# Performance work log

Measured on AMD Instinct MI355X. Metric: run time of the kernel, lower is better.

The kernel has to match this reference:

```python
import jax, jax.numpy as jnp
import numpy as np

B, L_VLM, L_EXP = 4, 768, 64
L_TOT = L_VLM + L_EXP
D_VLM, D_EXP = 2048, 1024
H, DH = 8, 256
ROPE_BASE = 10000.0
SCALE = 1.0 / np.sqrt(DH).astype(np.float32)


def setup_inputs() -> dict:
    key = jax.random.key(0)
    ks = jax.random.split(key, 12)
    s = 0.02  # weight init scale
    return {
        "vlm_hidden": jax.random.normal(ks[0], (B, L_VLM, D_VLM), jnp.float32),
        "exp_hidden": jax.random.normal(ks[1], (B, L_EXP, D_EXP), jnp.float32),
        "attention_mask": jnp.zeros((B, 1, L_TOT, L_TOT), jnp.float32),  # additive mask
        "position_ids": jnp.broadcast_to(jnp.arange(L_TOT, dtype=jnp.int32)[None, :], (B, L_TOT)),
        "wq_v": jax.random.normal(ks[2], (D_VLM, H * DH), jnp.float32) * s,
        "wk_v": jax.random.normal(ks[3], (D_VLM, H * DH), jnp.float32) * s,
        "wv_v": jax.random.normal(ks[4], (D_VLM, H * DH), jnp.float32) * s,
        "wo_v": jax.random.normal(ks[5], (H * DH, D_VLM), jnp.float32) * s,
        "wq_e": jax.random.normal(ks[6], (D_EXP, H * DH), jnp.float32) * s,
        "wk_e": jax.random.normal(ks[7], (D_EXP, H * DH), jnp.float32) * s,
        "wv_e": jax.random.normal(ks[8], (D_EXP, H * DH), jnp.float32) * s,
        "wo_e": jax.random.normal(ks[9], (H * DH, D_EXP), jnp.float32) * s,
    }


def _proj(hs, w):
    # [B, L, D] @ [D, H*DH] -> [B, H, L, DH]
    b, l, _ = hs.shape
    return jnp.einsum('bld,de->ble', hs, w).reshape(b, l, H, DH).transpose(0, 2, 1, 3)


def _rope(x, cos, sin):
    # NeoX-style rotate-half (Gemma / vLLM RotaryEmbedding with rotary_dim == head_dim)
    d2 = x.shape[-1] // 2
    x1, x2 = x[..., :d2], x[..., d2:]
    return jnp.concatenate([x1 * cos - x2 * sin, x2 * cos + x1 * sin], axis=-1)


def reference(vlm_hidden, exp_hidden, attention_mask, position_ids,
              wq_v, wk_v, wv_v, wo_v, wq_e, wk_e, wv_e, wo_e):
    # 1) separate per-stream Q/K/V projections, 2) concat along sequence dim
    q = jnp.concatenate([_proj(vlm_hidden, wq_v), _proj(exp_hidden, wq_e)], axis=2)
    k = jnp.concatenate([_proj(vlm_hidden, wk_v), _proj(exp_hidden, wk_e)], axis=2)
    v = jnp.concatenate([_proj(vlm_hidden, wv_v), _proj(exp_hidden, wv_e)], axis=2)

    # 3) rotary positional embedding on the joint sequence
    inv_freq = 1.0 / (ROPE_BASE ** (jnp.arange(0, DH, 2, dtype=jnp.float32) / DH))  # [DH/2]
    freqs = position_ids.astype(jnp.float32)[:, :, None] * inv_freq                 # [B, L, DH/2]
    cos = jnp.cos(freqs)[:, None]  # [B, 1, L, DH/2]
    sin = jnp.sin(freqs)[:, None]
    q = _rope(q, cos, sin)
    k = _rope(k, cos, sin)

    # 4) masked attention over the joint sequence
    scores = jnp.einsum('bhqd,bhkd->bhqk', q, k) * SCALE + attention_mask
    probs = jax.nn.softmax(scores, axis=-1)
    out = jnp.einsum('bhqk,bhkd->bhqd', probs, v)              # [B, H, L, DH]
    out = out.transpose(0, 2, 1, 3).reshape(B, L_TOT, H * DH)  # [B, L, H*DH]

    # 5) split back and apply per-stream output projections
    vlm_out = jnp.einsum('ble,ed->bld', out[:, :L_VLM], wo_v)
    exp_out = jnp.einsum('ble,ed->bld', out[:, L_VLM:], wo_e)
    return vlm_out, exp_out
```

## Files before the change

### kernel.cpp

```cpp
#include <hip/hip_runtime.h>

typedef unsigned short u16;
using bf16x8 = __attribute__((ext_vector_type(8))) __bf16;
using f32x4  = __attribute__((ext_vector_type(4))) float;

__device__ __forceinline__ u16 f2bf(float f) {
  unsigned u = __builtin_bit_cast(unsigned, f);
  u += 0x7FFFu + ((u >> 16) & 1u);
  return (u16)(u >> 16);
}
__device__ __forceinline__ float bf2f(u16 s) {
  unsigned u = ((unsigned)s) << 16;
  return __builtin_bit_cast(float, u);
}
__device__ __forceinline__ void lds16(const void* g, void* l) {
  __builtin_amdgcn_global_load_lds(
      (const __attribute__((address_space(1))) void*)g,
      (__attribute__((address_space(3))) void*)l, 16, 0, 0);
}

#define PH_SYNC() \
  __builtin_amdgcn_s_barrier(); \
  asm volatile("s_waitcnt lgkmcnt(0)" ::: "memory"); \
  __builtin_amdgcn_sched_barrier(0);

#define MFMA8(MA, MB) \
  __builtin_amdgcn_s_setprio(1); \
  acc[MA][0] = __builtin_amdgcn_mfma_f32_16x16x32_bf16(a0, b0, acc[MA][0], 0, 0, 0); \
  acc[MB][0] = __builtin_amdgcn_mfma_f32_16x16x32_bf16(a1, b0, acc[MB][0], 0, 0, 0); \
  acc[MA][1] = __builtin_amdgcn_mfma_f32_16x16x32_bf16(a0, b1, acc[MA][1], 0, 0, 0); \
  acc[MB][1] = __builtin_amdgcn_mfma_f32_16x16x32_bf16(a1, b1, acc[MB][1], 0, 0, 0); \
  acc[MA][2] = __builtin_amdgcn_mfma_f32_16x16x32_bf16(a0, b2, acc[MA][2], 0, 0, 0); \
  acc[MB][2] = __builtin_amdgcn_mfma_f32_16x16x32_bf16(a1, b2, acc[MB][2], 0, 0, 0); \
  acc[MA][3] = __builtin_amdgcn_mfma_f32_16x16x32_bf16(a0, b3, acc[MA][3], 0, 0, 0); \
  acc[MB][3] = __builtin_amdgcn_mfma_f32_16x16x32_bf16(a1, b3, acc[MB][3], 0, 0, 0); \
  __builtin_amdgcn_s_setprio(0);

__device__ __forceinline__ void gemm_dp(
    const u16* aR0, const u16* aR1, const u16* bR0, const u16* bR1,
    int NT, int t, u16* As, u16* Bs, f32x4 acc[4][4])
{
  const int lane = t & 63;
  const int fr = lane & 15;
  const int sA = ((lane >> 4) ^ ((fr >> 1) & 3)) << 3;
  const int offA = (((t >> 7) & 1) * 64 + fr) * 32 + sA;
  const int offB = (((t >> 6) & 1) * 64 + fr) * 32 + sA;

  lds16(aR0,      As + t * 8);
  lds16(aR1,      As + 2048 + t * 8);
  lds16(bR0,      Bs + t * 8);
  lds16(bR1,      Bs + 2048 + t * 8);
  lds16(aR0 + 32, As + 4096 + t * 8);
  lds16(aR1 + 32, As + 4096 + 2048 + t * 8);
  lds16(bR0 + 32, Bs + 4096 + t * 8);
  lds16(bR1 + 32, Bs + 4096 + 2048 + t * 8);
  lds16(bR0 + 64, Bs + 8192 + t * 8);
  lds16(bR1 + 64, Bs + 8192 + 2048 + t * 8);
  lds16(aR0 + 64, As + 8192 + t * 8);
  lds16(aR1 + 64, As + 8192 + 2048 + t * 8);
  lds16(bR0 + 96, Bs + 8192 + 4096 + t * 8);
  lds16(bR1 + 96, Bs + 8192 + 4096 + 2048 + t * 8);
  asm volatile("s_waitcnt vmcnt(10)" ::: "memory");
  __builtin_amdgcn_s_barrier();

  for (int T = 0; T < NT; ++T) {
    const int p = T & 1;
    u16* Ab = As + p * 8192;
    u16* Bb = Bs + p * 8192;
    u16* An = As + (p ^ 1) * 8192;
    const bool s1 = (T + 1 < NT), s2 = (T + 2 < NT);
    const int k1 = (T + 1) * 64, k2 = (T + 2) * 64;
    bf16x8 a0, a1, b0, b1, b2, b3;

    a0 = *(const bf16x8*)(Ab + offA);
    a1 = *(const bf16x8*)(Ab + offA + 512);
    b0 = *(const bf16x8*)(Bb + offB);
    b1 = *(const bf16x8*)(Bb + offB + 512);
    b2 = *(const bf16x8*)(Bb + offB + 1024);
    b3 = *(const bf16x8*)(Bb + offB + 1536);
    if (s1) {
      lds16(aR0 + k1 + 32, An + 4096 + t * 8);
      lds16(aR1 + k1 + 32, An + 4096 + 2048 + t * 8);
    }
    PH_SYNC();
    MFMA8(0, 1);
    __builtin_amdgcn_s_barrier();

    a0 = *(const bf16x8*)(Ab + offA + 1024);
    a1 = *(const bf16x8*)(Ab + offA + 1536);
    if (s2) {
      lds16(bR0 + k2, Bb + t * 8);
      lds16(bR1 + k2, Bb + 2048 + t * 8);
    }
    PH_SYNC();
    MFMA8(2, 3);
    if (s2) asm volatile("s_waitcnt vmcnt(10)" ::: "memory");
    else    asm volatile("s_waitcnt vmcnt(0)"  ::: "memory");
    __builtin_amdgcn_s_barrier();

    a0 = *(const bf16x8*)(Ab + offA + 4096);
    a1 = *(const bf16x8*)(Ab + offA + 4096 + 512);
    b0 = *(const bf16x8*)(Bb + offB + 4096);
    b1 = *(const bf16x8*)(Bb + offB + 4096 + 512);
    b2 = *(const bf16x8*)(Bb + offB + 4096 + 1024);
    b3 = *(const bf16x8*)(Bb + offB + 4096 + 1536);
    if (s2) {
      lds16(aR0 + k2, Ab + t * 8);
      lds16(aR1 + k2, Ab + 2048 + t * 8);
    }
    PH_SYNC();
    MFMA8(0, 1);
    __builtin_amdgcn_s_barrier();

    a0 = *(const bf16x8*)(Ab + offA + 4096 + 1024);
    a1 = *(const bf16x8*)(Ab + offA + 4096 + 1536);
    if (s2) {
      lds16(bR0 + k2 + 32, Bb + 4096 + t * 8);
      lds16(bR1 + k2 + 32, Bb + 4096 + 2048 + t * 8);
    }
    PH_SYNC();
    MFMA8(2, 3);
    if (s2) asm volatile("s_waitcnt vmcnt(10)" ::: "memory");
    else    asm volatile("s_waitcnt vmcnt(0)"  ::: "memory");
    __builtin_amdgcn_s_barrier();
  }
}

struct PrepArgs {
  const float* tsrc[8]; u16* tdst[8]; int tK[8]; int tN[8];
  const float* csrc[2]; u16* cdst[2]; int cn4[2];
};

__global__ __launch_bounds__(256) void g_prep(PrepArgs a)
{
  __shared__ float T[32][33];
  const int z = blockIdx.z;
  if (z < 8) {
    const int Krows = a.tK[z], Ncols = a.tN[z];
    const int k0 = blockIdx.y * 32, n0 = blockIdx.x * 32;
    if (k0 >= Krows || n0 >= Ncols) return;
    const float* W = a.tsrc[z];
    u16* Wt = a.tdst[z];
    const int tx = threadIdx.x & 31, ty = threadIdx.x >> 5;
#pragma unroll
    for (int r = 0; r < 4; ++r)
      T[ty + r * 8][tx] = W[(size_t)(k0 + ty + r * 8) * Ncols + n0 + tx];
    __syncthreads();
#pragma unroll
    for (int r = 0; r < 4; ++r)
      Wt[(size_t)(n0 + ty + r * 8) * Krows + k0 + tx] = f2bf(T[tx][ty + r * 8]);
  } else {
    const int j = z - 8;
    const int n4 = a.cn4[j];
    const float* X = a.csrc[j];
    u16* Y = a.cdst[j];
    const int blk = blockIdx.y * gridDim.x + blockIdx.x;
    const int stride = gridDim.x * gridDim.y * 256;
    for (int i = blk * 256 + threadIdx.x; i < n4; i += stride) {
      float4 f = ((const float4*)X)[i];
      ushort4 u;
      u.x = f2bf(f.x); u.y = f2bf(f.y); u.z = f2bf(f.z); u.w = f2bf(f.w);
      ((ushort4*)Y)[i] = u;
    }
  }
}

__global__ __launch_bounds__(256) void g_proj_qkv(
    const u16* __restrict__ Xv, const u16* __restrict__ Xe,
    const u16* __restrict__ Wv_cat, const u16* __restrict__ We_cat,
    u16* __restrict__ Qb, u16* __restrict__ Kb, u16* __restrict__ Vt)
{
  __shared__ __align__(16) u16 As[16384], Bs[16384];
  const int z = blockIdx.z;
  const u16* X; const u16* Wt; int Kdim, rows_pb, l_off;
  if (z == 0) { X = Xv; Wt = Wv_cat; Kdim = 2048; rows_pb = 768; l_off = 0; }
  else {
    if (blockIdx.y >= 2) return;
    X = Xe; Wt = We_cat; Kdim = 1024; rows_pb = 64; l_off = 768;
  }
  const int t = threadIdx.x;
  const int m0 = blockIdx.y * 128, n0 = blockIdx.x * 128;
  const int r0 = t >> 2;
  const int sw = ((t & 3) ^ ((t >> 3) & 3)) * 8;
  const u16* a0 = X + (size_t)(m0 + r0) * Kdim + sw;
  const u16* a1 = X + (size_t)(m0 + r0 + 64) * Kdim + sw;
  const u16* b0 = Wt + (size_t)(n0 + r0) * Kdim + sw;
  const u16* b1 = Wt + (size_t)(n0 + r0 + 64) * Kdim + sw;

  f32x4 acc[4][4] = {};
  gemm_dp(a0, a1, b0, b1, Kdim >> 6, t, As, Bs, acc);

  const int lane = t & 63;
  const int rbase = m0 + (t >> 7) * 64 + ((lane >> 4) << 2);
  const int cbase = n0 + ((t >> 6) & 1) * 64 + (lane & 15);
  const int sect = n0 >> 11;

  if (sect < 2) {
    u16* Out = (sect == 0) ? Qb : Kb;
#pragma unroll
    for (int mt = 0; mt < 4; ++mt) {
#pragma unroll
      for (int r = 0; r < 4; ++r) {
        int m = rbase + mt * 16 + r;
        int b = m / rows_pb;
        int l = m - b * rows_pb + l_off;
#pragma unroll
        for (int nt = 0; nt < 4; ++nt) {
          int nloc = (cbase + nt * 16) & 2047;
          Out[(((size_t)(b * 8 + (nloc >> 8))) * 832 + l) * 256 + (nloc & 255)] =
              f2bf(acc[mt][nt][r]);
        }
      }
    }
  } else {
#pragma unroll
    for (int mt = 0; mt < 4; ++mt) {
      int mb = rbase + mt * 16;
      int b = mb / rows_pb;
      int l = mb - b * rows_pb + l_off;
#pragma unroll
      for (int nt = 0; nt < 4; ++nt) {
        int nloc = (cbase + nt * 16) & 2047;
        ushort4 p;
        p.x = f2bf(acc[mt][nt][0]); p.y = f2bf(acc[mt][nt][1]);
        p.z = f2bf(acc[mt][nt][2]); p.w = f2bf(acc[mt][nt][3]);
        *(ushort4*)&Vt[(((size_t)(b * 8 + (nloc >> 8))) * 256 + (nloc & 255)) * 832 + l] = p;
      }
    }
  }
}

__global__ __launch_bounds__(128) void g_rope(
    u16* __restrict__ Q, u16* __restrict__ Kx, const int* __restrict__ pos)
{
  const int blk = blockIdx.x;
  const int l = blk % 832, bh = blk / 832, b = bh >> 3;
  const int i = threadIdx.x;
  const float p = (float)pos[b * 832 + l];
  const float inv = exp2f(-(float)i * 0.103810252965229910f);
  const float ang = p * inv;
  const float c = cosf(ang), s = sinf(ang);
  const size_t base = ((size_t)bh * 832 + l) * 256;

  float x1 = bf2f(Q[base + i]), x2 = bf2f(Q[base + i + 128]);
  Q[base + i]       = f2bf((x1 * c - x2 * s) * 0.0625f);
  Q[base + i + 128] = f2bf((x2 * c + x1 * s) * 0.0625f);
  x1 = bf2f(Kx[base + i]); x2 = bf2f(Kx[base + i + 128]);
  Kx[base + i]       = f2bf(x1 * c - x2 * s);
  Kx[base + i + 128] = f2bf(x2 * c + x1 * s);
}

__global__ __launch_bounds__(256) void g_flash(
    const u16* __restrict__ Qb, const u16* __restrict__ Kb,
    const u16* __restrict__ Vt, const float* __restrict__ mask,
    u16* __restrict__ AO)
{
  __shared__ __align__(16) u16 Ks[8192];
  __shared__ __align__(16) u16 Vs[8192];
  __shared__ __align__(16) u16 Ps[2048];
  const int t = threadIdx.x;
  const int lane = t & 63, w = t >> 6, quad = lane >> 4;
  const int wb = w * 512;

  const int id = blockIdx.x;
  const int x = id & 7, k = id >> 3;
  const int bh = x + 8 * (k / 13);
  const int q0 = (k % 13) * 64;
  const int b = bh >> 3, h = bh & 7;

  const u16* Ksrc = Kb + (size_t)bh * 832 * 256;
  const u16* Vsrc = Vt + (size_t)bh * 256 * 832;
  const float* Mrow = mask + (size_t)b * 832 * 832;

  bf16x8 qf[8];
#pragma unroll
  for (int kf = 0; kf < 8; ++kf)
    qf[kf] = *(const bf16x8*)(
        Qb + ((size_t)bh * 832 + q0 + w * 16 + (lane & 15)) * 256 +
        kf * 32 + quad * 8);

  float mrun[4], lrun[4];
#pragma unroll
  for (int r = 0; r < 4; ++r) { mrun[r] = -3e38f; lrun[r] = 0.f; }
  f32x4 oa[16] = {};

  for (int kt = 0; kt < 26; ++kt) {
    __syncthreads();
#pragma unroll
    for (int p = 0; p < 4; ++p) {
      int c = p * 256 + t;
      int row = c >> 5, chk = c & 31;
      lds16(Ksrc + (size_t)(kt * 32 + row) * 256 + ((chk ^ (row & 7)) * 8),
            Ks + c * 8);
    }
#pragma unroll
    for (int p = 0; p < 4; ++p) {
      int c = p * 256 + t;
      int row = c >> 3;
      int lc = (c & 7) ^ (row & 7);
      int dh = 2 * row + (lc >> 2);
      lds16(Vsrc + (size_t)dh * 832 + kt * 32 + (lc & 3) * 8, Vs + c * 8);
    }
    __syncthreads();

    f32x4 sa[2] = {};
#pragma unroll
    for (int ks = 0; ks < 8; ++ks)
#pragma unroll
      for (int nt = 0; nt < 2; ++nt) {
        int krow = nt * 16 + (lane & 15);
        bf16x8 kb = *(const bf16x8*)(
            Ks + krow * 256 + (((ks * 4 + quad) ^ (krow & 7)) * 8));
        sa[nt] = __builtin_amdgcn_mfma_f32_16x16x32_bf16(qf[ks], kb, sa[nt], 0, 0, 0);
      }

    float alpha[4];
#pragma unroll
    for (int r = 0; r < 4; ++r) {
      int prow = quad * 4 + r;
      int q = q0 + w * 16 + prow;
      const float* mrp = Mrow + (size_t)q * 832 + kt * 32 + (lane & 15);
      float v0 = sa[0][r] + mrp[0];
      float v1 = sa[1][r] + mrp[16];
      float mx = fmaxf(v0, v1);
      mx = fmaxf(mx, __shfl_xor(mx, 1));
      mx = fmaxf(mx, __shfl_xor(mx, 2));
      mx = fmaxf(mx, __shfl_xor(mx, 4));
      mx = fmaxf(mx, __shfl_xor(mx, 8));
      float mn = fmaxf(mrun[r], mx);
      float al = __expf(mrun[r] - mn);
      float p0 = __expf(v0 - mn), p1 = __expf(v1 - mn);
      float rs = p0 + p1;
      rs += __shfl_xor(rs, 1);
      rs += __shfl_xor(rs, 2);
      rs += __shfl_xor(rs, 4);
      rs += __shfl_xor(rs, 8);
      lrun[r] = lrun[r] * al + rs;
      mrun[r] = mn;
      alpha[r] = al;
      int s0 = ((lane >> 3) & 1) ^ quad;
      int s1 = (2 | ((lane >> 3) & 1)) ^ quad;
      Ps[wb + prow * 32 + s0 * 8 + (lane & 7)] = f2bf(p0);
      Ps[wb + prow * 32 + s1 * 8 + (lane & 7)] = f2bf(p1);
    }

#pragma unroll
    for (int nt = 0; nt < 16; ++nt)
#pragma unroll
      for (int r = 0; r < 4; ++r) oa[nt][r] *= alpha[r];

    int prow2 = lane & 15;
    bf16x8 pa = *(const bf16x8*)(
        Ps + wb + prow2 * 32 + ((quad ^ ((prow2 >> 2) & 3)) * 8));
#pragma unroll
    for (int nt = 0; nt < 16; ++nt) {
      int dh = nt * 16 + (lane & 15);
      int row = dh >> 1;
      int lc = ((dh & 1) << 2) | quad;
      bf16x8 vb = *(const bf16x8*)(Vs + row * 64 + ((lc ^ (row & 7)) * 8));
      oa[nt] = __builtin_amdgcn_mfma_f32_16x16x32_bf16(pa, vb, oa[nt], 0, 0, 0);
    }
  }

  float linv[4];
#pragma unroll
  for (int r = 0; r < 4; ++r) linv[r] = 1.0f / lrun[r];
#pragma unroll
  for (int r = 0; r < 4; ++r) {
    size_t l = q0 + w * 16 + quad * 4 + r;
    u16* dst = AO + ((size_t)b * 832 + l) * 2048 + h * 256 + (lane & 15);
#pragma unroll
    for (int nt = 0; nt < 16; ++nt)
      dst[nt * 16] = f2bf(oa[nt][r] * linv[r]);
  }
}

__global__ __launch_bounds__(256) void g_oproj2(
    const u16* __restrict__ AO, const u16* __restrict__ Wov,
    const u16* __restrict__ Woe, float* __restrict__ out)
{
  __shared__ __align__(16) u16 As[16384], Bs[16384];
  const int z = blockIdx.z;
  const u16* Wt; float* C; int N, rows_pb, l_off;
  if (z == 0) { Wt = Wov; C = out; N = 2048; rows_pb = 768; l_off = 0; }
  else {
    if (blockIdx.y >= 2 || blockIdx.x >= 8) return;
    Wt = Woe; C = out + (size_t)4 * 768 * 2048; N = 1024; rows_pb = 64; l_off = 768;
  }
  const int t = threadIdx.x;
  const int m0 = blockIdx.y * 128, n0 = blockIdx.x * 128;
  const int r0 = t >> 2;
  const int sw = ((t & 3) ^ ((t >> 3) & 3)) * 8;
  int mr0 = m0 + r0, mr1 = m0 + r0 + 64;
  int ba = mr0 / rows_pb, bb = mr1 / rows_pb;
  const u16* a0 = AO + ((size_t)ba * 832 + (mr0 - ba * rows_pb) + l_off) * 2048 + sw;
  const u16* a1 = AO + ((size_t)bb * 832 + (mr1 - bb * rows_pb) + l_off) * 2048 + sw;
  const u16* b0 = Wt + (size_t)(n0 + r0) * 2048 + sw;
  const u16* b1 = Wt + (size_t)(n0 + r0 + 64) * 2048 + sw;

  f32x4 acc[4][4] = {};
  gemm_dp(a0, a1, b0, b1, 32, t, As, Bs, acc);

  const int lane = t & 63;
  const int rbase = m0 + (t >> 7) * 64 + ((lane >> 4) << 2);
  const int cbase = n0 + ((t >> 6) & 1) * 64 + (lane & 15);
#pragma unroll
  for (int mt = 0; mt < 4; ++mt)
#pragma unroll
    for (int r = 0; r < 4; ++r) {
      size_t m = rbase + mt * 16 + r;
#pragma unroll
      for (int nt = 0; nt < 4; ++nt)
        C[m * N + cbase + nt * 16] = acc[mt][nt][r];
    }
}

extern "C" void kernel_launch(void* const* d_in, const int* in_sizes, int n_in,
                              void* d_out, int out_size, void* d_ws, size_t ws_size,
                              hipStream_t stream)
{
  const float* vlm_h = (const float*)d_in[0];
  const float* exp_h = (const float*)d_in[1];
  const float* mask  = (const float*)d_in[2];
  const int*   pos   = (const int*)d_in[3];
  const float* wq_v  = (const float*)d_in[4];
  const float* wk_v  = (const float*)d_in[5];
  const float* wv_v  = (const float*)d_in[6];
  const float* wo_v  = (const float*)d_in[7];
  const float* wq_e  = (const float*)d_in[8];
  const float* wk_e  = (const float*)d_in[9];
  const float* wv_e  = (const float*)d_in[10];
  const float* wo_e  = (const float*)d_in[11];
  float* out = (float*)d_out;

  u16* U = (u16*)d_ws;
  u16* Xv   = U; U += (size_t)4 * 768 * 2048;
  u16* Xe   = U; U += (size_t)4 * 64 * 1024;
  u16* Wcv  = U; U += (size_t)6144 * 2048;
  u16* Wce  = U; U += (size_t)6144 * 1024;
  u16* Wov  = U; U += (size_t)2048 * 2048;
  u16* Woe  = U; U += (size_t)1024 * 2048;
  u16* Qb   = U; U += (size_t)32 * 832 * 256;
  u16* Kb   = U; U += (size_t)32 * 832 * 256;
  u16* Vt   = U; U += (size_t)32 * 256 * 832;
  u16* AO   = U; U += (size_t)4 * 832 * 2048;

  const dim3 blk(256);

  PrepArgs pa;
  pa.tsrc[0] = wq_v; pa.tdst[0] = Wcv;                        pa.tK[0] = 2048; pa.tN[0] = 2048;
  pa.tsrc[1] = wk_v; pa.tdst[1] = Wcv + (size_t)2048 * 2048;  pa.tK[1] = 2048; pa.tN[1] = 2048;
  pa.tsrc[2] = wv_v; pa.tdst[2] = Wcv + (size_t)4096 * 2048;  pa.tK[2] = 2048; pa.tN[2] = 2048;
  pa.tsrc[3] = wo_v; pa.tdst[3] = Wov;                        pa.tK[3] = 2048; pa.tN[3] = 2048;
  pa.tsrc[4] = wq_e; pa.tdst[4] = Wce;                        pa.tK[4] = 1024; pa.tN[4] = 2048;
  pa.tsrc[5] = wk_e; pa.tdst[5] = Wce + (size_t)2048 * 1024;  pa.tK[5] = 1024; pa.tN[5] = 2048;
  pa.tsrc[6] = wv_e; pa.tdst[6] = Wce + (size_t)4096 * 1024;  pa.tK[6] = 1024; pa.tN[6] = 2048;
  pa.tsrc[7] = wo_e; pa.tdst[7] = Woe;                        pa.tK[7] = 2048; pa.tN[7] = 1024;
  pa.csrc[0] = vlm_h; pa.cdst[0] = Xv; pa.cn4[0] = 1572864;
  pa.csrc[1] = exp_h; pa.cdst[1] = Xe; pa.cn4[1] = 65536;
  g_prep<<<dim3(64, 64, 10), blk, 0, stream>>>(pa);

  g_proj_qkv<<<dim3(48, 24, 2), blk, 0, stream>>>(Xv, Xe, Wcv, Wce, Qb, Kb, Vt);

  g_rope<<<dim3(32 * 832), dim3(128), 0, stream>>>(Qb, Kb, pos);

  g_flash<<<dim3(416), blk, 0, stream>>>(Qb, Kb, Vt, mask, AO);

  g_oproj2<<<dim3(16, 24, 2), blk, 0, stream>>>(AO, Wov, Woe, out);
}
```

Measured before the change: 445.6 us.

## Use 256x256 tiles with 8-wave pipelined GEMM for QKV projection

Replaces the 128x128 tile, 4-wave QKV projection GEMM with a 256x256 tile, 512-thread kernel. It double-buffers K=64 halves in LDS and interleaves global-to-LDS staging with MFMA phases separated by barriers. The larger tile raises arithmetic intensity and cuts redundant global loads of X and W. In exchange it uses 128KB of LDS per block and far fewer blocks, which risks a tail or occupancy imbalance on the MI355X's many CUs. The expert stream now uses a single 256-row block per batch slice.

```diff
diff --git a/kernel.cpp b/kernel.cpp
--- a/kernel.cpp
+++ b/kernel.cpp
@@ -19,6 +19,122 @@
       (__attribute__((address_space(3))) void*)l, 16, 0, 0);
 }
 
+#define MM(A, B, C) __builtin_amdgcn_mfma_f32_16x16x32_bf16(A, B, C, 0, 0, 0)
+
+#define PH_TOP() \
+  __builtin_amdgcn_s_barrier(); \
+  asm volatile("s_waitcnt lgkmcnt(0)" ::: "memory"); \
+  __builtin_amdgcn_sched_barrier(0);
+
+#define LOADA(Abase, QD) \
+  a00 = *(const bf16x8*)((Abase) + (2*(QD))*1024 + cA0); \
+  a01 = *(const bf16x8*)((Abase) + (2*(QD))*1024 + cA1); \
+  a10 = *(const bf16x8*)((Abase) + (2*(QD)+1)*1024 + cA0); \
+  a11 = *(const bf16x8*)((Abase) + (2*(QD)+1)*1024 + cA1);
+
+#define LOADB(Bbase) \
+  b00 = *(const bf16x8*)((Bbase) + cA0);        b01 = *(const bf16x8*)((Bbase) + cA1); \
+  b10 = *(const bf16x8*)((Bbase) + 1024 + cA0); b11 = *(const bf16x8*)((Bbase) + 1024 + cA1); \
+  b20 = *(const bf16x8*)((Bbase) + 2048 + cA0); b21 = *(const bf16x8*)((Bbase) + 2048 + cA1); \
+  b30 = *(const bf16x8*)((Bbase) + 3072 + cA0); b31 = *(const bf16x8*)((Bbase) + 3072 + cA1);
+
+#define DOMFMA(M0, M1) \
+  __builtin_amdgcn_s_setprio(1); \
+  acc[M0][0] = MM(a00, b00, acc[M0][0]); \
+  acc[M0][1] = MM(a00, b10, acc[M0][1]); \
+  acc[M0][2] = MM(a00, b20, acc[M0][2]); \
+  acc[M0][3] = MM(a00, b30, acc[M0][3]); \
+  acc[M1][0] = MM(a10, b00, acc[M1][0]); \
+  acc[M1][1] = MM(a10, b10, acc[M1][1]); \
+  acc[M1][2] = MM(a10, b20, acc[M1][2]); \
+  acc[M1][3] = MM(a10, b30, acc[M1][3]); \
+  acc[M0][0] = MM(a01, b01, acc[M0][0]); \
+  acc[M0][1] = MM(a01, b11, acc[M0][1]); \
+  acc[M0][2] = MM(a01, b21, acc[M0][2]); \
+  acc[M0][3] = MM(a01, b31, acc[M0][3]); \
+  acc[M1][0] = MM(a11, b01, acc[M1][0]); \
+  acc[M1][1] = MM(a11, b11, acc[M1][1]); \
+  acc[M1][2] = MM(a11, b21, acc[M1][2]); \
+  acc[M1][3] = MM(a11, b31, acc[M1][3]); \
+  __builtin_amdgcn_s_setprio(0);
+
+#define STG_A(BUF, H, KOFF) \
+  lds16(pA[(H)*2+0] + (KOFF), As + (BUF)*16384 + (H)*8192 + t*8); \
+  lds16(pA[(H)*2+1] + (KOFF), As + (BUF)*16384 + (H)*8192 + 4096 + t*8);
+#define STG_B(BUF, H, KOFF) \
+  lds16(pB[(H)*2+0] + (KOFF), Bs + (BUF)*16384 + (H)*8192 + t*8); \
+  lds16(pB[(H)*2+1] + (KOFF), Bs + (BUF)*16384 + (H)*8192 + 4096 + t*8);
+
+__device__ __forceinline__ void gemm256(
+    const u16* const pA[4], const u16* const pB[4],
+    int NIter, int t, u16* As, u16* Bs, f32x4 (&acc)[8][4])
+{
+  const int lane = t & 63, fr = lane & 15, q4 = lane >> 4;
+  const int wn = (t >> 6) & 3, wm = t >> 8;
+  const int cA0 = fr * 64 + ((q4 ^ (fr & 7)) * 8);
+  const int cA1 = fr * 64 + (((4 + q4) ^ (fr & 7)) * 8);
+  const u16* Ard0 = As + wm * 8192;
+  const u16* Ard1 = As + 16384 + wm * 8192;
+  const u16* Brd0 = Bs + (wn >> 1) * 8192 + (wn & 1) * 4096;
+  const u16* Brd1 = Brd0 + 16384;
+
+  STG_A(0, 0, 0); STG_A(0, 1, 0);
+  STG_B(0, 0, 0); STG_B(0, 1, 0);
+  STG_B(1, 0, 64); STG_B(1, 1, 64);
+  asm volatile("s_waitcnt vmcnt(4)" ::: "memory");
+  __builtin_amdgcn_s_barrier();
+
+  for (int it = 0; it < NIter; ++it) {
+    const bool s = (it + 1 < NIter);
+    const int kT1 = (2 * it + 1) * 64;
+    const int kT2 = (2 * it + 2) * 64;
+    const int kT3 = (2 * it + 3) * 64;
+    bf16x8 a00, a01, a10, a11, b00, b01, b10, b11, b20, b21, b30, b31;
+
+    LOADB(Brd0); LOADA(Ard0, 0);
+    STG_A(1, 0, kT1); STG_A(1, 1, kT1);
+    PH_TOP(); DOMFMA(0, 1);
+    __builtin_amdgcn_s_barrier();
+
+    LOADA(Ard0, 1);
+    if (s) { STG_B(0, 0, kT2); }
+    PH_TOP(); DOMFMA(2, 3);
+    __builtin_amdgcn_s_barrier();
+
+    LOADA(Ard0, 2);
+    if (s) { STG_B(0, 1, kT2); }
+    PH_TOP(); DOMFMA(4, 5);
+    __builtin_amdgcn_s_barrier();
+
+    LOADA(Ard0, 3);
+    PH_TOP(); DOMFMA(6, 7);
+    if (s) { asm volatile("s_waitcnt vmcnt(4)" ::: "memory"); }
+    else   { asm volatile("s_waitcnt vmcnt(0)" ::: "memory"); }
+    __builtin_amdgcn_s_barrier();
+
+    LOADB(Brd1); LOADA(Ard1, 0);
+    if (s) { STG_A(0, 0, kT2); }
+    PH_TOP(); DOMFMA(0, 1);
+    __builtin_amdgcn_s_barrier();
+
+    LOADA(Ard1, 1);
+    if (s) { STG_A(0, 1, kT2); }
+    PH_TOP(); DOMFMA(2, 3);
+    __builtin_amdgcn_s_barrier();
+
+    LOADA(Ard1, 2);
+    if (s) { STG_B(1, 0, kT3); }
+    PH_TOP(); DOMFMA(4, 5);
+    __builtin_amdgcn_s_barrier();
+
+    LOADA(Ard1, 3);
+    if (s) { STG_B(1, 1, kT3); }
+    PH_TOP(); DOMFMA(6, 7);
+    if (s) { asm volatile("s_waitcnt vmcnt(4)" ::: "memory"); }
+    __builtin_amdgcn_s_barrier();
+  }
+}
+
 #define PH_SYNC() \
   __builtin_amdgcn_s_barrier(); \
   asm volatile("s_waitcnt lgkmcnt(0)" ::: "memory"); \
@@ -26,14 +142,14 @@
 
 #define MFMA8(MA, MB) \
   __builtin_amdgcn_s_setprio(1); \
-  acc[MA][0] = __builtin_amdgcn_mfma_f32_16x16x32_bf16(a0, b0, acc[MA][0], 0, 0, 0); \
-  acc[MB][0] = __builtin_amdgcn_mfma_f32_16x16x32_bf16(a1, b0, acc[MB][0], 0, 0, 0); \
-  acc[MA][1] = __builtin_amdgcn_mfma_f32_16x16x32_bf16(a0, b1, acc[MA][1], 0, 0, 0); \
-  acc[MB][1] = __builtin_amdgcn_mfma_f32_16x16x32_bf16(a1, b1, acc[MB][1], 0, 0, 0); \
-  acc[MA][2] = __builtin_amdgcn_mfma_f32_16x16x32_bf16(a0, b2, acc[MA][2], 0, 0, 0); \
-  acc[MB][2] = __builtin_amdgcn_mfma_f32_16x16x32_bf16(a1, b2, acc[MB][2], 0, 0, 0); \
-  acc[MA][3] = __builtin_amdgcn_mfma_f32_16x16x32_bf16(a0, b3, acc[MA][3], 0, 0, 0); \
-  acc[MB][3] = __builtin_amdgcn_mfma_f32_16x16x32_bf16(a1, b3, acc[MB][3], 0, 0, 0); \
+  acc[MA][0] = MM(a0, b0, acc[MA][0]); \
+  acc[MB][0] = MM(a1, b0, acc[MB][0]); \
+  acc[MA][1] = MM(a0, b1, acc[MA][1]); \
+  acc[MB][1] = MM(a1, b1, acc[MB][1]); \
+  acc[MA][2] = MM(a0, b2, acc[MA][2]); \
+  acc[MB][2] = MM(a1, b2, acc[MB][2]); \
+  acc[MA][3] = MM(a0, b3, acc[MA][3]); \
+  acc[MB][3] = MM(a1, b3, acc[MB][3]); \
   __builtin_amdgcn_s_setprio(0);
 
 __device__ __forceinline__ void gemm_dp(
@@ -165,40 +281,43 @@
   }
 }
 
-__global__ __launch_bounds__(256) void g_proj_qkv(
+__global__ __launch_bounds__(512, 2) void g_proj_qkv(
     const u16* __restrict__ Xv, const u16* __restrict__ Xe,
     const u16* __restrict__ Wv_cat, const u16* __restrict__ We_cat,
     u16* __restrict__ Qb, u16* __restrict__ Kb, u16* __restrict__ Vt)
 {
-  __shared__ __align__(16) u16 As[16384], Bs[16384];
+  __shared__ __align__(16) u16 As[32768], Bs[32768];
   const int z = blockIdx.z;
   const u16* X; const u16* Wt; int Kdim, rows_pb, l_off;
   if (z == 0) { X = Xv; Wt = Wv_cat; Kdim = 2048; rows_pb = 768; l_off = 0; }
   else {
-    if (blockIdx.y >= 2) return;
+    if (blockIdx.y >= 1) return;
     X = Xe; Wt = We_cat; Kdim = 1024; rows_pb = 64; l_off = 768;
   }
   const int t = threadIdx.x;
-  const int m0 = blockIdx.y * 128, n0 = blockIdx.x * 128;
-  const int r0 = t >> 2;
-  const int sw = ((t & 3) ^ ((t >> 3) & 3)) * 8;
-  const u16* a0 = X + (size_t)(m0 + r0) * Kdim + sw;
-  const u16* a1 = X + (size_t)(m0 + r0 + 64) * Kdim + sw;
-  const u16* b0 = Wt + (size_t)(n0 + r0) * Kdim + sw;
-  const u16* b1 = Wt + (size_t)(n0 + r0 + 64) * Kdim + sw;
-
-  f32x4 acc[4][4] = {};
-  gemm_dp(a0, a1, b0, b1, Kdim >> 6, t, As, Bs, acc);
-
-  const int lane = t & 63;
-  const int rbase = m0 + (t >> 7) * 64 + ((lane >> 4) << 2);
-  const int cbase = n0 + ((t >> 6) & 1) * 64 + (lane & 15);
+  const int m0 = blockIdx.y * 256, n0 = blockIdx.x * 256;
+  const int rr = t >> 3;
+  const int swz = ((t & 7) ^ (rr & 7)) * 8;
+  const u16* pA[4]; const u16* pB[4];
+#pragma unroll
+  for (int q = 0; q < 4; ++q) {
+    pA[q] = X  + (size_t)(m0 + rr + 64 * q) * Kdim + swz;
+    pB[q] = Wt + (size_t)(n0 + rr + 64 * q) * Kdim + swz;
+  }
+
+  f32x4 acc[8][4] = {};
+  gemm256(pA, pB, Kdim >> 7, t, As, Bs, acc);
+
+  const int lane = t & 63, q4 = lane >> 4;
+  const int wn = (t >> 6) & 3, wm = t >> 8;
+  const int rbase = m0 + wm * 128 + q4 * 4;
+  const int cbase = n0 + wn * 64 + (lane & 15);
   const int sect = n0 >> 11;
 
   if (sect < 2) {
     u16* Out = (sect == 0) ? Qb : Kb;
 #pragma unroll
-    for (int mt = 0; mt < 4; ++mt) {
+    for (int mt = 0; mt < 8; ++mt) {
 #pragma unroll
       for (int r = 0; r < 4; ++r) {
         int m = rbase + mt * 16 + r;
@@ -214,7 +333,7 @@
     }
   } else {
 #pragma unroll
-    for (int mt = 0; mt < 4; ++mt) {
+    for (int mt = 0; mt < 8; ++mt) {
       int mb = rbase + mt * 16;
       int b = mb / rows_pb;
       int l = mb - b * rows_pb + l_off;
@@ -460,7 +579,7 @@
   pa.csrc[1] = exp_h; pa.cdst[1] = Xe; pa.cn4[1] = 65536;
   g_prep<<<dim3(64, 64, 10), blk, 0, stream>>>(pa);
 
-  g_proj_qkv<<<dim3(48, 24, 2), blk, 0, stream>>>(Xv, Xe, Wcv, Wce, Qb, Kb, Vt);
+  g_proj_qkv<<<dim3(24, 12, 2), dim3(512), 0, stream>>>(Xv, Xe, Wcv, Wce, Qb, Kb, Vt);
 
   g_rope<<<dim3(32 * 832), dim3(128), 0, stream>>>(Qb, Kb, pos);
 
```

New measurement: 427.3 us. 4.1% less time.
